# Kernel optimization log

Measured on AMD Instinct MI355X. Metric: run time of the kernel, lower is better.

## Reference

```python
import jax, jax.numpy as jnp
import numpy as np

TOKENS = 8192
MODEL_DIM = 4096
NUM_EXPERTS = 64
K = 2


def setup_inputs() -> dict:
    key = jax.random.key(0)
    kx, kw = jax.random.split(key)
    x = jax.random.normal(kx, (TOKENS, MODEL_DIM), dtype=jnp.float32)
    # nn.Linear default init: U(-1/sqrt(fan_in), 1/sqrt(fan_in)); weight shape [E, D]
    bound = 1.0 / np.sqrt(MODEL_DIM)
    W = jax.random.uniform(kw, (NUM_EXPERTS, MODEL_DIM), dtype=jnp.float32,
                           minval=-bound, maxval=bound)
    return {"x": x, "W": W}


def reference(x, W):
    # TopKGate.forward with k=2, eval mode (no noise): logits -> top2gating
    logits = jnp.einsum("td,ed->te", x.astype(jnp.float32), W)  # [T, E]
    # topk indices (sorted by value, like torch.topk)
    _, topi = jax.lax.top_k(logits, K)                           # [T, K]
    gates = jax.nn.softmax(logits, axis=-1)                      # [T, E]
    # (gates * one_hot(idx)).sum(-1) == gather of gates at idx
    g = jnp.take_along_axis(gates, topi, axis=-1)                # [T, K]
    eps = jnp.finfo(gates.dtype).eps
    denom = jnp.maximum(jnp.sum(g, axis=-1, keepdims=True), eps)
    g = g / denom
    # matches return ([idx1, idx2], [gate1, gate2]) with flattened indices
    return (topi[:, 0], topi[:, 1], g[:, 0], g[:, 1])
```

## Files before the change

kernel.cpp:

```cpp
#include <hip/hip_runtime.h>
#include <float.h>
#include <math.h>

#define TOKENS 8192
#define DIM    4096

typedef _Float16 v8h  __attribute__((ext_vector_type(8)));
typedef float    v4f  __attribute__((ext_vector_type(4)));

typedef __attribute__((address_space(3))) unsigned int lds_uint;
typedef const __attribute__((address_space(1))) unsigned int glob_uint;

__device__ __forceinline__ void stage16(const _Float16* g, _Float16* l) {
    __builtin_amdgcn_global_load_lds((glob_uint*)g, (lds_uint*)l, 16, 0, 0);
}

__global__ __launch_bounds__(256) void prep_w_kernel(
    const float* __restrict__ W, _Float16* __restrict__ WF) {
    int n = blockIdx.x * 256 + threadIdx.x;
    int chunk = n >> 8;
    int et    = (n >> 6) & 3;
    int lane  = n & 63;
    int e  = et * 16 + (lane & 15);
    int k0 = chunk * 32 + (lane >> 4) * 8;
    const float* src = W + (size_t)e * DIM + k0;
    v8h h, l;
    #pragma unroll
    for (int j = 0; j < 8; ++j) {
        float w = src[j];
        _Float16 wh = (_Float16)w;
        h[j] = wh;
        l[j] = (_Float16)((w - (float)wh) * 2048.0f);
    }
    size_t base = (size_t)chunk * 4096 + (size_t)et * 512 + (size_t)lane * 8;
    *(v8h*)(WF + base)        = h;
    *(v8h*)(WF + base + 2048) = l;
}

#define LOAD_A4(A0a, A0b, A1a, A1b, jj) do {                                  \
    const float* ap_ = abase + (jj) * 32;                                     \
    A0a = *(const v4f*)(ap_);       A0b = *(const v4f*)(ap_ + 4);             \
    A1a = *(const v4f*)(ap_ + 32);  A1b = *(const v4f*)(ap_ + 36);            \
} while (0)

#define STAGE2(BI, jj) do {                                                   \
    stage16(sbase + (size_t)(jj) * 4096,       &buf[BI][wq * 1024]);          \
    stage16(sbase + (size_t)(jj) * 4096 + 512, &buf[BI][wq * 1024 + 512]);    \
} while (0)

#define CVT1(f, j) {                                                          \
    _Float16 h_ = (_Float16)(f);                                              \
    ah[j] = h_;                                                               \
    al[j] = (_Float16)(((f) - (float)h_) * 2048.0f);                          \
}
#define CVT(Aa, Ab) do {                                                      \
    CVT1(Aa[0], 0) CVT1(Aa[1], 1) CVT1(Aa[2], 2) CVT1(Aa[3], 3)               \
    CVT1(Ab[0], 4) CVT1(Ab[1], 5) CVT1(Ab[2], 6) CVT1(Ab[3], 7)               \
} while (0)

#define MFMA16(a, b, c) __builtin_amdgcn_mfma_f32_16x16x32_f16(a, b, c, 0, 0, 0)

#define COMPC(BI, COFF, Aa, Ab) do {                                          \
    CVT(Aa, Ab);                                                              \
    const _Float16* bp_ = &buf[BI][COFF] + (size_t)lane * 8;                  \
    v8h h0_ = *(const v8h*)(bp_);                                             \
    v8h h1_ = *(const v8h*)(bp_ + 512);                                       \
    v8h h2_ = *(const v8h*)(bp_ + 1024);                                      \
    v8h h3_ = *(const v8h*)(bp_ + 1536);                                      \
    v8h l0_ = *(const v8h*)(bp_ + 2048);                                      \
    v8h l1_ = *(const v8h*)(bp_ + 2560);                                      \
    v8h l2_ = *(const v8h*)(bp_ + 3072);                                      \
    v8h l3_ = *(const v8h*)(bp_ + 3584);                                      \
    acc1[0] = MFMA16(ah, h0_, acc1[0]);                                       \
    acc1[1] = MFMA16(ah, h1_, acc1[1]);                                       \
    acc1[2] = MFMA16(ah, h2_, acc1[2]);                                       \
    acc1[3] = MFMA16(ah, h3_, acc1[3]);                                       \
    acc2[0] = MFMA16(al, h0_, acc2[0]);  acc2[0] = MFMA16(ah, l0_, acc2[0]);  \
    acc2[1] = MFMA16(al, h1_, acc2[1]);  acc2[1] = MFMA16(ah, l1_, acc2[1]);  \
    acc2[2] = MFMA16(al, h2_, acc2[2]);  acc2[2] = MFMA16(ah, l2_, acc2[2]);  \
    acc2[3] = MFMA16(al, h3_, acc2[3]);  acc2[3] = MFMA16(ah, l3_, acc2[3]);  \
} while (0)

#define BARRIER_KEEP(n) do {                                                  \
    __builtin_amdgcn_sched_barrier(0);                                        \
    asm volatile("s_waitcnt vmcnt(" #n ")" ::: "memory");                     \
    __builtin_amdgcn_sched_barrier(0);                                        \
    __builtin_amdgcn_s_barrier();                                             \
    __builtin_amdgcn_sched_barrier(0);                                        \
} while (0)

#define ITER_FULL(i, BI, BN, Ac0a, Ac0b, Ac1a, Ac1b) do {                     \
    STAGE2(BN, 2 * (i) + 4);                                                  \
    COMPC(BI, 0,    Ac0a, Ac0b);                                              \
    COMPC(BI, 4096, Ac1a, Ac1b);                                              \
    LOAD_A4(Ac0a, Ac0b, Ac1a, Ac1b, 2 * (i) + 4);                             \
    BARRIER_KEEP(10);                                                         \
} while (0)

__global__ __launch_bounds__(512, 4) void logits_kernel(
    const float* __restrict__ x,
    const _Float16* __restrict__ WF,
    float* __restrict__ P) {

    __shared__ _Float16 buf[3][8192];

    const int tid  = threadIdx.x;
    const int wq   = tid >> 6;
    const int lane = tid & 63;
    const int kg   = (int)(blockIdx.x & 7);
    const int tg   = (int)(blockIdx.x >> 3);
    const int tok0 = tg * 128 + wq * 16;
    const int art  = lane & 15;
    const int akg  = lane >> 4;
    const int chunk0 = kg * 16;

    const float*    abase = x  + (size_t)(tok0 + art) * DIM + chunk0 * 32 + akg * 8;
    const _Float16* sbase = WF + (size_t)chunk0 * 4096 + wq * 1024 + lane * 8;

    v4f acc1[4], acc2[4];
    #pragma unroll
    for (int e4 = 0; e4 < 4; ++e4) { acc1[e4] = (v4f)0.0f; acc2[e4] = (v4f)0.0f; }

    v4f S0c0a, S0c0b, S0c1a, S0c1b;
    v4f S1c0a, S1c0b, S1c1a, S1c1b;
    v8h ah, al;

    STAGE2(0, 0);
    LOAD_A4(S0c0a, S0c0b, S0c1a, S0c1b, 0);
    STAGE2(1, 2);
    LOAD_A4(S1c0a, S1c0b, S1c1a, S1c1b, 2);
    BARRIER_KEEP(10);

    ITER_FULL(0, 0, 2, S0c0a, S0c0b, S0c1a, S0c1b);
    ITER_FULL(1, 1, 0, S1c0a, S1c0b, S1c1a, S1c1b);
    ITER_FULL(2, 2, 1, S0c0a, S0c0b, S0c1a, S0c1b);
    ITER_FULL(3, 0, 2, S1c0a, S1c0b, S1c1a, S1c1b);
    ITER_FULL(4, 1, 0, S0c0a, S0c0b, S0c1a, S0c1b);
    ITER_FULL(5, 2, 1, S1c0a, S1c0b, S1c1a, S1c1b);
    COMPC(0, 0,    S0c0a, S0c0b);
    COMPC(0, 4096, S0c1a, S0c1b);
    BARRIER_KEEP(4);
    COMPC(1, 0,    S1c0a, S1c0b);
    COMPC(1, 4096, S1c1a, S1c1b);

    const float inv2048 = 1.0f / 2048.0f;
    #pragma unroll
    for (int e4 = 0; e4 < 4; ++e4) {
        #pragma unroll
        for (int r = 0; r < 4; ++r) {
            float v = acc1[e4][r] + acc2[e4][r] * inv2048;
            P[((size_t)kg * TOKENS + tok0 + akg * 4 + r) * 64 + e4 * 16 + art] = v;
        }
    }
}

__global__ __launch_bounds__(256) void reduce_topk_kernel(
    const float* __restrict__ P, float* __restrict__ out) {
    const int wq   = threadIdx.x >> 6;
    const int lane = threadIdx.x & 63;
    #pragma unroll
    for (int tt = 0; tt < 4; ++tt) {
        int gt = blockIdx.x * 16 + wq * 4 + tt;
        float v = 0.f;
        #pragma unroll
        for (int kg = 0; kg < 8; ++kg)
            v += P[((size_t)kg * TOKENS + gt) * 64 + lane];

        float bv = v; int bi = lane;
        #pragma unroll
        for (int off = 32; off >= 1; off >>= 1) {
            float ov = __shfl_xor(bv, off);
            int   oi = __shfl_xor(bi, off);
            if (ov > bv || (ov == bv && oi < bi)) { bv = ov; bi = oi; }
        }
        float v2 = (lane == bi) ? -FLT_MAX : v;
        float bv2 = v2; int bi2 = lane;
        #pragma unroll
        for (int off = 32; off >= 1; off >>= 1) {
            float ov = __shfl_xor(bv2, off);
            int   oi = __shfl_xor(bi2, off);
            if (ov > bv2 || (ov == bv2 && oi < bi2)) { bv2 = ov; bi2 = oi; }
        }

        if (lane == 0) {
            float g0 = 1.0f / (1.0f + expf(bv2 - bv));
            out[gt]              = (float)bi;
            out[TOKENS + gt]     = (float)bi2;
            out[2 * TOKENS + gt] = g0;
            out[3 * TOKENS + gt] = 1.0f - g0;
        }
    }
}

extern "C" void kernel_launch(void* const* d_in, const int* in_sizes, int n_in,
                              void* d_out, int out_size, void* d_ws, size_t ws_size,
                              hipStream_t stream) {
    const float* x = (const float*)d_in[0];
    const float* W = (const float*)d_in[1];
    float* out     = (float*)d_out;
    _Float16* WF   = (_Float16*)d_ws;
    float* P       = (float*)((char*)d_ws + (1 << 20));

    prep_w_kernel<<<128, 256, 0, stream>>>(W, WF);
    logits_kernel<<<512, 512, 0, stream>>>(x, WF, P);
    reduce_topk_kernel<<<512, 256, 0, stream>>>(P, out);
}
```

Baseline: 43.24 us.

## Give each wave 32 tokens to reuse staged W fragments across two MFMA tiles

The logits kernel now runs 4 waves of 256 threads per block instead of 8. Each wave computes two 16-token tiles, so every LDS read of the W hi/lo fragments feeds both tiles. The LDS buffers shrink to one 32-wide k chunk per stage, and the pipeline runs 16 stages instead of 8. The goal is fewer LDS reads per MFMA and a lower staging cost per wave, at the price of more accumulator registers, fewer resident waves and a longer serial pipeline with more barriers.

```diff
diff --git a/kernel.cpp b/kernel.cpp
--- a/kernel.cpp
+++ b/kernel.cpp
@@ -37,48 +37,47 @@
     *(v8h*)(WF + base + 2048) = l;
 }
 
-#define LOAD_A4(A0a, A0b, A1a, A1b, jj) do {                                  \
-    const float* ap_ = abase + (jj) * 32;                                     \
-    A0a = *(const v4f*)(ap_);       A0b = *(const v4f*)(ap_ + 4);             \
-    A1a = *(const v4f*)(ap_ + 32);  A1b = *(const v4f*)(ap_ + 36);            \
-} while (0)
-
-#define STAGE2(BI, jj) do {                                                   \
-    stage16(sbase + (size_t)(jj) * 4096,       &buf[BI][wq * 1024]);          \
-    stage16(sbase + (size_t)(jj) * 4096 + 512, &buf[BI][wq * 1024 + 512]);    \
-} while (0)
-
-#define CVT1(f, j) {                                                          \
+#define LOAD_A4(A0a, A0b, A1a, A1b, cc) do {                                  \
+    const float* a0_ = abase0 + (cc) * 32;                                    \
+    const float* a1_ = abase1 + (cc) * 32;                                    \
+    A0a = *(const v4f*)(a0_);  A0b = *(const v4f*)(a0_ + 4);                  \
+    A1a = *(const v4f*)(a1_);  A1b = *(const v4f*)(a1_ + 4);                  \
+} while (0)
+
+#define STAGE(BI, cc) do {                                                    \
+    stage16(sbase + (size_t)(cc) * 4096,       &buf[BI][wq * 1024]);          \
+    stage16(sbase + (size_t)(cc) * 4096 + 512, &buf[BI][wq * 1024 + 512]);    \
+} while (0)
+
+#define CVT1(dsth, dstl, f, j) {                                              \
     _Float16 h_ = (_Float16)(f);                                              \
-    ah[j] = h_;                                                               \
-    al[j] = (_Float16)(((f) - (float)h_) * 2048.0f);                          \
-}
-#define CVT(Aa, Ab) do {                                                      \
-    CVT1(Aa[0], 0) CVT1(Aa[1], 1) CVT1(Aa[2], 2) CVT1(Aa[3], 3)               \
-    CVT1(Ab[0], 4) CVT1(Ab[1], 5) CVT1(Ab[2], 6) CVT1(Ab[3], 7)               \
+    dsth[j] = h_;                                                             \
+    dstl[j] = (_Float16)(((f) - (float)h_) * 2048.0f);                        \
+}
+#define CVT(dsth, dstl, Aa, Ab) do {                                          \
+    CVT1(dsth, dstl, Aa[0], 0) CVT1(dsth, dstl, Aa[1], 1)                     \
+    CVT1(dsth, dstl, Aa[2], 2) CVT1(dsth, dstl, Aa[3], 3)                     \
+    CVT1(dsth, dstl, Ab[0], 4) CVT1(dsth, dstl, Ab[1], 5)                     \
+    CVT1(dsth, dstl, Ab[2], 6) CVT1(dsth, dstl, Ab[3], 7)                     \
 } while (0)
 
 #define MFMA16(a, b, c) __builtin_amdgcn_mfma_f32_16x16x32_f16(a, b, c, 0, 0, 0)
 
-#define COMPC(BI, COFF, Aa, Ab) do {                                          \
-    CVT(Aa, Ab);                                                              \
-    const _Float16* bp_ = &buf[BI][COFF] + (size_t)lane * 8;                  \
-    v8h h0_ = *(const v8h*)(bp_);                                             \
-    v8h h1_ = *(const v8h*)(bp_ + 512);                                       \
-    v8h h2_ = *(const v8h*)(bp_ + 1024);                                      \
-    v8h h3_ = *(const v8h*)(bp_ + 1536);                                      \
-    v8h l0_ = *(const v8h*)(bp_ + 2048);                                      \
-    v8h l1_ = *(const v8h*)(bp_ + 2560);                                      \
-    v8h l2_ = *(const v8h*)(bp_ + 3072);                                      \
-    v8h l3_ = *(const v8h*)(bp_ + 3584);                                      \
-    acc1[0] = MFMA16(ah, h0_, acc1[0]);                                       \
-    acc1[1] = MFMA16(ah, h1_, acc1[1]);                                       \
-    acc1[2] = MFMA16(ah, h2_, acc1[2]);                                       \
-    acc1[3] = MFMA16(ah, h3_, acc1[3]);                                       \
-    acc2[0] = MFMA16(al, h0_, acc2[0]);  acc2[0] = MFMA16(ah, l0_, acc2[0]);  \
-    acc2[1] = MFMA16(al, h1_, acc2[1]);  acc2[1] = MFMA16(ah, l1_, acc2[1]);  \
-    acc2[2] = MFMA16(al, h2_, acc2[2]);  acc2[2] = MFMA16(ah, l2_, acc2[2]);  \
-    acc2[3] = MFMA16(al, h3_, acc2[3]);  acc2[3] = MFMA16(ah, l3_, acc2[3]);  \
+#define COMPC(BI, A0a, A0b, A1a, A1b) do {                                    \
+    CVT(ah0, al0, A0a, A0b);                                                  \
+    CVT(ah1, al1, A1a, A1b);                                                  \
+    const _Float16* bp_ = &buf[BI][0] + (size_t)lane * 8;                     \
+    _Pragma("unroll")                                                         \
+    for (int e4_ = 0; e4_ < 4; ++e4_) {                                       \
+        v8h h_ = *(const v8h*)(bp_ + e4_ * 512);                              \
+        v8h l_ = *(const v8h*)(bp_ + 2048 + e4_ * 512);                       \
+        acc1[e4_] = MFMA16(ah0, h_, acc1[e4_]);                               \
+        acc3[e4_] = MFMA16(ah1, h_, acc3[e4_]);                               \
+        acc2[e4_] = MFMA16(al0, h_, acc2[e4_]);                               \
+        acc2[e4_] = MFMA16(ah0, l_, acc2[e4_]);                               \
+        acc4[e4_] = MFMA16(al1, h_, acc4[e4_]);                               \
+        acc4[e4_] = MFMA16(ah1, l_, acc4[e4_]);                               \
+    }                                                                         \
 } while (0)
 
 #define BARRIER_KEEP(n) do {                                                  \
@@ -89,67 +88,78 @@
     __builtin_amdgcn_sched_barrier(0);                                        \
 } while (0)
 
-#define ITER_FULL(i, BI, BN, Ac0a, Ac0b, Ac1a, Ac1b) do {                     \
-    STAGE2(BN, 2 * (i) + 4);                                                  \
-    COMPC(BI, 0,    Ac0a, Ac0b);                                              \
-    COMPC(BI, 4096, Ac1a, Ac1b);                                              \
-    LOAD_A4(Ac0a, Ac0b, Ac1a, Ac1b, 2 * (i) + 4);                             \
+#define ITER_FULL(c, BI, BN, Ac0a, Ac0b, Ac1a, Ac1b) do {                     \
+    STAGE(BN, (c) + 2);                                                       \
+    COMPC(BI, Ac0a, Ac0b, Ac1a, Ac1b);                                        \
+    LOAD_A4(Ac0a, Ac0b, Ac1a, Ac1b, (c) + 2);                                 \
     BARRIER_KEEP(10);                                                         \
 } while (0)
 
-__global__ __launch_bounds__(512, 4) void logits_kernel(
+__global__ __launch_bounds__(256, 2) void logits_kernel(
     const float* __restrict__ x,
     const _Float16* __restrict__ WF,
     float* __restrict__ P) {
 
-    __shared__ _Float16 buf[3][8192];
+    __shared__ _Float16 buf[3][4096];
 
     const int tid  = threadIdx.x;
     const int wq   = tid >> 6;
     const int lane = tid & 63;
     const int kg   = (int)(blockIdx.x & 7);
     const int tg   = (int)(blockIdx.x >> 3);
-    const int tok0 = tg * 128 + wq * 16;
+    const int tokB = tg * 128 + wq * 32;
     const int art  = lane & 15;
     const int akg  = lane >> 4;
     const int chunk0 = kg * 16;
 
-    const float*    abase = x  + (size_t)(tok0 + art) * DIM + chunk0 * 32 + akg * 8;
+    const float* abase0 = x + (size_t)(tokB + art) * DIM      + chunk0 * 32 + akg * 8;
+    const float* abase1 = x + (size_t)(tokB + 16 + art) * DIM + chunk0 * 32 + akg * 8;
     const _Float16* sbase = WF + (size_t)chunk0 * 4096 + wq * 1024 + lane * 8;
 
-    v4f acc1[4], acc2[4];
-    #pragma unroll
-    for (int e4 = 0; e4 < 4; ++e4) { acc1[e4] = (v4f)0.0f; acc2[e4] = (v4f)0.0f; }
-
-    v4f S0c0a, S0c0b, S0c1a, S0c1b;
-    v4f S1c0a, S1c0b, S1c1a, S1c1b;
-    v8h ah, al;
-
-    STAGE2(0, 0);
-    LOAD_A4(S0c0a, S0c0b, S0c1a, S0c1b, 0);
-    STAGE2(1, 2);
-    LOAD_A4(S1c0a, S1c0b, S1c1a, S1c1b, 2);
+    v4f acc1[4], acc2[4], acc3[4], acc4[4];
+    #pragma unroll
+    for (int e4 = 0; e4 < 4; ++e4) {
+        acc1[e4] = (v4f)0.0f; acc2[e4] = (v4f)0.0f;
+        acc3[e4] = (v4f)0.0f; acc4[e4] = (v4f)0.0f;
+    }
+
+    v4f S0a, S0b, S0c, S0d;
+    v4f S1a, S1b, S1c, S1d;
+    v8h ah0, al0, ah1, al1;
+
+    STAGE(0, 0);
+    LOAD_A4(S0a, S0b, S0c, S0d, 0);
+    STAGE(1, 1);
+    LOAD_A4(S1a, S1b, S1c, S1d, 1);
     BARRIER_KEEP(10);
 
-    ITER_FULL(0, 0, 2, S0c0a, S0c0b, S0c1a, S0c1b);
-    ITER_FULL(1, 1, 0, S1c0a, S1c0b, S1c1a, S1c1b);
-    ITER_FULL(2, 2, 1, S0c0a, S0c0b, S0c1a, S0c1b);
-    ITER_FULL(3, 0, 2, S1c0a, S1c0b, S1c1a, S1c1b);
-    ITER_FULL(4, 1, 0, S0c0a, S0c0b, S0c1a, S0c1b);
-    ITER_FULL(5, 2, 1, S1c0a, S1c0b, S1c1a, S1c1b);
-    COMPC(0, 0,    S0c0a, S0c0b);
-    COMPC(0, 4096, S0c1a, S0c1b);
+    ITER_FULL(0,  0, 2, S0a, S0b, S0c, S0d);
+    ITER_FULL(1,  1, 0, S1a, S1b, S1c, S1d);
+    ITER_FULL(2,  2, 1, S0a, S0b, S0c, S0d);
+    ITER_FULL(3,  0, 2, S1a, S1b, S1c, S1d);
+    ITER_FULL(4,  1, 0, S0a, S0b, S0c, S0d);
+    ITER_FULL(5,  2, 1, S1a, S1b, S1c, S1d);
+    ITER_FULL(6,  0, 2, S0a, S0b, S0c, S0d);
+    ITER_FULL(7,  1, 0, S1a, S1b, S1c, S1d);
+    ITER_FULL(8,  2, 1, S0a, S0b, S0c, S0d);
+    ITER_FULL(9,  0, 2, S1a, S1b, S1c, S1d);
+    ITER_FULL(10, 1, 0, S0a, S0b, S0c, S0d);
+    ITER_FULL(11, 2, 1, S1a, S1b, S1c, S1d);
+    ITER_FULL(12, 0, 2, S0a, S0b, S0c, S0d);
+    ITER_FULL(13, 1, 0, S1a, S1b, S1c, S1d);
+    COMPC(2, S0a, S0b, S0c, S0d);
     BARRIER_KEEP(4);
-    COMPC(1, 0,    S1c0a, S1c0b);
-    COMPC(1, 4096, S1c1a, S1c1b);
+    COMPC(0, S1a, S1b, S1c, S1d);
 
     const float inv2048 = 1.0f / 2048.0f;
     #pragma unroll
     for (int e4 = 0; e4 < 4; ++e4) {
         #pragma unroll
         for (int r = 0; r < 4; ++r) {
-            float v = acc1[e4][r] + acc2[e4][r] * inv2048;
-            P[((size_t)kg * TOKENS + tok0 + akg * 4 + r) * 64 + e4 * 16 + art] = v;
+            float v0 = acc1[e4][r] + acc2[e4][r] * inv2048;
+            float v1 = acc3[e4][r] + acc4[e4][r] * inv2048;
+            P[((size_t)kg * TOKENS + tokB + akg * 4 + r) * 64 + e4 * 16 + art]      = v0;
+            P[((size_t)kg * TOKENS + tokB + 16 + akg * 4 + r) * 64 + e4 * 16 + art] = v1;
         }
     }
 }
@@ -202,6 +212,6 @@
     float* P       = (float*)((char*)d_ws + (1 << 20));
 
     prep_w_kernel<<<128, 256, 0, stream>>>(W, WF);
-    logits_kernel<<<512, 512, 0, stream>>>(x, WF, P);
+    logits_kernel<<<512, 256, 0, stream>>>(x, WF, P);
     reduce_topk_kernel<<<512, 256, 0, stream>>>(P, out);
 }
```

New measurement: 41.19 us. 1.05x faster.
